# Optimization experiments

Hardware: AMD Instinct MI355X
Metric: run time of the kernel (lower is better)

The kernel has to match this reference:

```python
import jax, jax.numpy as jnp
import numpy as np

FEATURES = 4096
BATCH = 2048


def setup_inputs() -> dict:
    key = jax.random.key(0)
    kx, kk = jax.random.split(key)
    x = jax.random.normal(kx, (BATCH, FEATURES), dtype=jnp.float32)
    kernel = jax.random.normal(kk, (FEATURES,), dtype=jnp.float32)
    return {"x": x, "kernel": kernel}


def reference(x, kernel):
    n = kernel.shape[0]
    i = jnp.arange(n)[:, None]   # [n,1]
    j = jnp.arange(n)[None, :]   # [1,n]
    idx = i - j                   # Toeplitz offsets
    # W[i,j] = kernel[i-j] if i>=j else 0  (causal lower-triangular Toeplitz)
    W = jnp.where(idx >= 0, kernel[jnp.clip(idx, 0, n - 1)], 0.0)
    # out[b,i] = sum_{j<=i} x[b,j] * kernel[i-j]  == x @ W.T
    return x @ W.T
```

## Files before the change

### kernel.cpp

```cpp
#include <hip/hip_runtime.h>
#include <hip/hip_bf16.h>


typedef unsigned short u16;
typedef __attribute__((ext_vector_type(8))) short  bf16x8;
typedef __attribute__((ext_vector_type(8))) unsigned short u16x8;
typedef __attribute__((ext_vector_type(4))) float  f32x4;

#define KDIM 4096
#define NDIM 4096
#define MDIM 2048
#define KREV_STRIDE 4608
#define KREV_BYTES  (8 * KREV_STRIDE * 2)
#define BSTRIDE 456
#define BBUF    (8 * BSTRIDE)

static __device__ inline u16 f2bf(float f) {
  unsigned u = __builtin_bit_cast(unsigned, f);
  unsigned r = u + 0x7FFFu + ((u >> 16) & 1u);
  return (u16)(r >> 16);
}

static __device__ inline void async_copy16(const void* g, void* l) {
  __builtin_amdgcn_global_load_lds((const __attribute__((address_space(1))) void*)g,
                                   (__attribute__((address_space(3))) void*)l,
                                   16, 0, 0);
}

__global__ __launch_bounds__(256) void prep(const float* __restrict__ x,
                                            const float* __restrict__ kern,
                                            u16* __restrict__ xb,
                                            u16* __restrict__ krevs,
                                            int conv_blocks) {
  int kb = (int)blockIdx.x - conv_blocks;
  if (kb >= 0) {
    int u = kb * 256 + threadIdx.x;
    for (int a = 0; a < 8; ++a) {
      int t = u + a - 8;
      u16 v = 0;
      if (t >= 0 && t <= 4095) v = f2bf(kern[4095 - t]);
      krevs[a * KREV_STRIDE + u] = v;
    }
  } else {
    size_t i = ((size_t)blockIdx.x * 256 + threadIdx.x) * 8;
    const f32x4* p = (const f32x4*)(x + i);
    f32x4 v0 = p[0], v1 = p[1];
    u16x8 r;
    r[0] = f2bf(v0[0]); r[1] = f2bf(v0[1]); r[2] = f2bf(v0[2]); r[3] = f2bf(v0[3]);
    r[4] = f2bf(v1[0]); r[5] = f2bf(v1[1]); r[6] = f2bf(v1[2]); r[7] = f2bf(v1[3]);
    *(u16x8*)(xb + i) = r;
  }
}

template <bool CONV>
__global__ __launch_bounds__(512, 4) void toeplitz_gemm(const void* __restrict__ Av,
                                                        const u16* __restrict__ krevs,
                                                        float* __restrict__ out) {
  __shared__ __align__(16) char smem_raw[80128];
  u16*   A_all = (u16*)smem_raw;
  u16*   B_all = (u16*)(smem_raw + 65536);
  f32x4* ep    = (f32x4*)smem_raw;

  const int tid  = threadIdx.x;
  const int w    = tid >> 6;
  const int g    = w >> 2;
  const int wl   = w & 3;
  const int lane = tid & 63;
  const int lane16 = lane & 15;
  const int quad   = lane >> 4;
  const int wm = wl >> 1;
  const int wn = wl & 1;

  const int b  = (int)blockIdx.x;
  const int x_ = b & 7;
  const int jj = b >> 3;
  const int mt = x_ + 8 * (jj & 1);
  const int ct = 31 - (jj >> 1);
  const int n0 = ct * 128;
  const int m0 = mt * 128;
  const int W  = 3968 - n0;

  int boff[4];
  for (int fn = 0; fn < 4; ++fn) {
    int n_g = n0 + wn * 64 + fn * 16 + lane16;
    int s0  = 4095 - n_g + quad * 8;
    int a   = s0 & 7;
    boff[fn] = a * BSTRIDE + (s0 - a + 8 - W);
  }

  f32x4 acc[4][4] = {};
  const int srow8 = lane >> 3;
  const int ssrc  = ((lane & 7) ^ srow8) * 8;

  const u16*  xb = (const u16*)Av;
  const float* xf = (const float*)Av;

  auto stageA = [&](int t) {
    const int k0 = t * 128 + g * 64;
    u16* A_dst = A_all + (((g << 1) | (t & 1)) << 13);
    if constexpr (CONV) {
      int j    = tid & 255;
      int row  = j >> 1;
      int lh   = j & 1;
      for (int lc = 0; lc < 4; ++lc) {
        int l = lh * 4 + lc;
        int p = l ^ (row & 7);
        const f32x4* px = (const f32x4*)(xf + (size_t)(m0 + row) * KDIM + k0 + l * 8);
        f32x4 v0 = px[0], v1 = px[1];
        u16x8 r;
        r[0]=f2bf(v0[0]); r[1]=f2bf(v0[1]); r[2]=f2bf(v0[2]); r[3]=f2bf(v0[3]);
        r[4]=f2bf(v1[0]); r[5]=f2bf(v1[1]); r[6]=f2bf(v1[2]); r[7]=f2bf(v1[3]);
        *(u16x8*)(&A_dst[row * 64 + p * 8]) = r;
      }
    } else {
      for (int c = 0; c < 4; ++c) {
        int g8  = c * 4 + wl;
        int row = g8 * 8 + srow8;
        async_copy16(xb + (size_t)(m0 + row) * KDIM + k0 + ssrc,
                     &A_dst[g8 * 512]);
      }
    }
  };
  auto stageB = [&](int c) {
    if (lane < 56)
      async_copy16(krevs + w * KREV_STRIDE + W + c * 256 + (lane << 3),
                   &B_all[(c & 1) * BBUF + w * BSTRIDE]);
  };

  stageB(0);
  stageA(0);
  asm volatile("s_waitcnt vmcnt(0) lgkmcnt(0)" ::: "memory");
  __builtin_amdgcn_s_barrier();
  asm volatile("" ::: "memory");

  const int cmax = ct >> 1;
  for (int t = 0; ; ++t) {
    if (t < ct) {
      stageA(t + 1);
      if (!(t & 1) && ((t >> 1) + 1) <= cmax) stageB((t >> 1) + 1);
    }
    const u16* Bb  = B_all + ((t >> 1) & 1) * BBUF;
    const u16* A_g = A_all + (((g << 1) | (t & 1)) << 13);
    const int  ksl = (t & 1) * 128 + g * 64;
    for (int kk = 0; kk < 2; ++kk) {
      bf16x8 af[4];
      const int p = (kk * 4 + quad) ^ (lane16 & 7);
      for (int fm = 0; fm < 4; ++fm) {
        int row = wm * 64 + fm * 16 + lane16;
        af[fm] = *(const bf16x8*)(&A_g[row * 64 + p * 8]);
      }
      bf16x8 bf[4];
      for (int fn = 0; fn < 4; ++fn)
        bf[fn] = *(const bf16x8*)(&Bb[boff[fn] + ksl + kk * 32]);
      __builtin_amdgcn_s_setprio(1);
      for (int fm = 0; fm < 4; ++fm)
        for (int fn = 0; fn < 4; ++fn)
          acc[fm][fn] = __builtin_amdgcn_mfma_f32_16x16x32_bf16(af[fm], bf[fn], acc[fm][fn], 0, 0, 0);
      __builtin_amdgcn_s_setprio(0);
    }
    if (t == ct) break;
    asm volatile("s_waitcnt vmcnt(0) lgkmcnt(0)" ::: "memory");
    __builtin_amdgcn_s_barrier();
    asm volatile("" ::: "memory");
  }

  const int j = tid & 255;
  for (int r = 0; r < 2; ++r) {
    __syncthreads();
    if (g == 1) {
      for (int fm2 = 0; fm2 < 2; ++fm2)
        for (int fn = 0; fn < 4; ++fn)
          ep[j * 9 + fm2 * 4 + fn] = acc[r * 2 + fm2][fn];
    }
    __syncthreads();
    if (g == 0) {
      for (int fm2 = 0; fm2 < 2; ++fm2)
        for (int fn = 0; fn < 4; ++fn)
          acc[r * 2 + fm2][fn] += ep[j * 9 + fm2 * 4 + fn];
    }
  }

  if (g == 0) {
    for (int fm = 0; fm < 4; ++fm) {
      int row_base = m0 + wm * 64 + fm * 16 + quad * 4;
      for (int fn = 0; fn < 4; ++fn) {
        int col = n0 + wn * 64 + fn * 16 + lane16;
        for (int r = 0; r < 4; ++r)
          out[(size_t)(row_base + r) * NDIM + col] = acc[fm][fn][r];
      }
    }
  }
}

extern "C" void kernel_launch(void* const* d_in, const int* in_sizes, int n_in,
                              void* d_out, int out_size, void* d_ws, size_t ws_size,
                              hipStream_t stream) {
  const float* x    = (const float*)d_in[0];
  const float* kern = (const float*)d_in[1];
  float* out = (float*)d_out;

  u16* krevs = (u16*)d_ws;
  u16* xb    = (u16*)((char*)d_ws + KREV_BYTES);
  const size_t need_fast = (size_t)KREV_BYTES + (size_t)MDIM * KDIM * 2;

  if (ws_size >= need_fast) {
    prep<<<4096 + 18, 256, 0, stream>>>(x, kern, xb, krevs, 4096);
    toeplitz_gemm<false><<<512, 512, 0, stream>>>(xb, krevs, out);
  } else {
    prep<<<18, 256, 0, stream>>>(x, kern, xb, krevs, 0);
    toeplitz_gemm<true><<<512, 512, 0, stream>>>(x, krevs, out);
  }
}
```

Measured before the change: 120.3 us.

## Pre-swizzle x into MFMA fragment layout and load A directly from global

The prep kernel now writes bf16 x in a fragment-major order so each lane's 16-byte A operand is contiguous. The GEMM drops LDS staging of A and loads A fragments straight from global/L2 into registers. This shrinks shared memory, which can raise occupancy, and halves the barrier count by syncing only on B buffer swaps. Block-to-tile ordering also interleaves long and short causal tiles for load balance, and setprio is removed. The trade-off is that the global load latency of A is now exposed on every step without software prefetch.

```diff
diff --git a/kernel.cpp b/kernel.cpp
--- a/kernel.cpp
+++ b/kernel.cpp
@@ -15,6 +15,8 @@
 #define BSTRIDE 456
 #define BBUF    (8 * BSTRIDE)
 
+#define MFMA_BF16 __builtin_amdgcn_mfma_f32_16x16x32_bf16
+
 static __device__ inline u16 f2bf(float f) {
   unsigned u = __builtin_bit_cast(unsigned, f);
   unsigned r = u + 0x7FFFu + ((u >> 16) & 1u);
@@ -32,9 +34,9 @@
                                             u16* __restrict__ xb,
                                             u16* __restrict__ krevs,
                                             int conv_blocks) {
-  int kb = (int)blockIdx.x - conv_blocks;
-  if (kb >= 0) {
-    int u = kb * 256 + threadIdx.x;
+  int kblk = (int)blockIdx.x - conv_blocks;
+  if (kblk >= 0) {
+    int u = kblk * 256 + threadIdx.x;
     for (int a = 0; a < 8; ++a) {
       int t = u + a - 8;
       u16 v = 0;
@@ -42,13 +44,18 @@
       krevs[a * KREV_STRIDE + u] = v;
     }
   } else {
-    size_t i = ((size_t)blockIdx.x * 256 + threadIdx.x) * 8;
-    const f32x4* p = (const f32x4*)(x + i);
+    unsigned tg  = blockIdx.x * 256 + threadIdx.x;
+    unsigned l   = tg & 63;
+    unsigned kb  = (tg >> 6) & 127;
+    unsigned rg  = tg >> 13;
+    unsigned row = rg * 16 + (l & 15);
+    unsigned k   = kb * 32 + (l >> 4) * 8;
+    const f32x4* p = (const f32x4*)(x + (size_t)row * KDIM + k);
     f32x4 v0 = p[0], v1 = p[1];
     u16x8 r;
     r[0] = f2bf(v0[0]); r[1] = f2bf(v0[1]); r[2] = f2bf(v0[2]); r[3] = f2bf(v0[3]);
     r[4] = f2bf(v1[0]); r[5] = f2bf(v1[1]); r[6] = f2bf(v1[2]); r[7] = f2bf(v1[3]);
-    *(u16x8*)(xb + i) = r;
+    *(u16x8*)(xb + (size_t)tg * 8) = r;
   }
 }
 
@@ -56,9 +63,8 @@
 __global__ __launch_bounds__(512, 4) void toeplitz_gemm(const void* __restrict__ Av,
                                                         const u16* __restrict__ krevs,
                                                         float* __restrict__ out) {
-  __shared__ __align__(16) char smem_raw[80128];
-  u16*   A_all = (u16*)smem_raw;
-  u16*   B_all = (u16*)(smem_raw + 65536);
+  __shared__ __align__(16) char smem_raw[36864];
+  u16*   B_all = (u16*)smem_raw;
   f32x4* ep    = (f32x4*)smem_raw;
 
   const int tid  = threadIdx.x;
@@ -74,8 +80,10 @@
   const int b  = (int)blockIdx.x;
   const int x_ = b & 7;
   const int jj = b >> 3;
-  const int mt = x_ + 8 * (jj & 1);
-  const int ct = 31 - (jj >> 1);
+  const int q  = jj & 31;
+  const int h  = jj >> 5;
+  const int mt = x_ + 8 * (q & 1);
+  const int ct = h ? (q >> 1) : 31 - (q >> 1);
   const int n0 = ct * 128;
   const int m0 = mt * 128;
   const int W  = 3968 - n0;
@@ -89,38 +97,16 @@
   }
 
   f32x4 acc[4][4] = {};
-  const int srow8 = lane >> 3;
-  const int ssrc  = ((lane & 7) ^ srow8) * 8;
-
-  const u16*  xb = (const u16*)Av;
-  const float* xf = (const float*)Av;
-
-  auto stageA = [&](int t) {
-    const int k0 = t * 128 + g * 64;
-    u16* A_dst = A_all + (((g << 1) | (t & 1)) << 13);
-    if constexpr (CONV) {
-      int j    = tid & 255;
-      int row  = j >> 1;
-      int lh   = j & 1;
-      for (int lc = 0; lc < 4; ++lc) {
-        int l = lh * 4 + lc;
-        int p = l ^ (row & 7);
-        const f32x4* px = (const f32x4*)(xf + (size_t)(m0 + row) * KDIM + k0 + l * 8);
-        f32x4 v0 = px[0], v1 = px[1];
-        u16x8 r;
-        r[0]=f2bf(v0[0]); r[1]=f2bf(v0[1]); r[2]=f2bf(v0[2]); r[3]=f2bf(v0[3]);
-        r[4]=f2bf(v1[0]); r[5]=f2bf(v1[1]); r[6]=f2bf(v1[2]); r[7]=f2bf(v1[3]);
-        *(u16x8*)(&A_dst[row * 64 + p * 8]) = r;
-      }
-    } else {
-      for (int c = 0; c < 4; ++c) {
-        int g8  = c * 4 + wl;
-        int row = g8 * 8 + srow8;
-        async_copy16(xb + (size_t)(m0 + row) * KDIM + k0 + ssrc,
-                     &A_dst[g8 * 512]);
-      }
-    }
-  };
+
+  const u16*   xb2 = (const u16*)Av;
+  const float* xf  = (const float*)Av;
+  const u16* pA[4];
+  if constexpr (!CONV) {
+    for (int fm = 0; fm < 4; ++fm)
+      pA[fm] = xb2 + (size_t)(mt * 8 + wm * 4 + fm) * 65536 + g * 1024 + lane * 8;
+  }
+  const int rowb = m0 + wm * 64 + lane16;
+
   auto stageB = [&](int c) {
     if (lane < 56)
       async_copy16(krevs + w * KREV_STRIDE + W + c * 256 + (lane << 3),
@@ -128,40 +114,47 @@
   };
 
   stageB(0);
-  stageA(0);
   asm volatile("s_waitcnt vmcnt(0) lgkmcnt(0)" ::: "memory");
   __builtin_amdgcn_s_barrier();
   asm volatile("" ::: "memory");
 
   const int cmax = ct >> 1;
   for (int t = 0; ; ++t) {
-    if (t < ct) {
-      stageA(t + 1);
-      if (!(t & 1) && ((t >> 1) + 1) <= cmax) stageB((t >> 1) + 1);
-    }
+    if (!(t & 1) && ((t >> 1) + 1) <= cmax) stageB((t >> 1) + 1);
+
     const u16* Bb  = B_all + ((t >> 1) & 1) * BBUF;
-    const u16* A_g = A_all + (((g << 1) | (t & 1)) << 13);
     const int  ksl = (t & 1) * 128 + g * 64;
+#pragma unroll
     for (int kk = 0; kk < 2; ++kk) {
       bf16x8 af[4];
-      const int p = (kk * 4 + quad) ^ (lane16 & 7);
-      for (int fm = 0; fm < 4; ++fm) {
-        int row = wm * 64 + fm * 16 + lane16;
-        af[fm] = *(const bf16x8*)(&A_g[row * 64 + p * 8]);
+      if constexpr (!CONV) {
+        const int eo = t * 2048 + kk * 512;
+        for (int fm = 0; fm < 4; ++fm)
+          af[fm] = *(const bf16x8*)(pA[fm] + eo);
+      } else {
+        const int k0 = t * 128 + g * 64 + kk * 32 + quad * 8;
+        for (int fm = 0; fm < 4; ++fm) {
+          const f32x4* px = (const f32x4*)(xf + (size_t)(rowb + fm * 16) * KDIM + k0);
+          f32x4 v0 = px[0], v1 = px[1];
+          u16x8 r;
+          r[0]=f2bf(v0[0]); r[1]=f2bf(v0[1]); r[2]=f2bf(v0[2]); r[3]=f2bf(v0[3]);
+          r[4]=f2bf(v1[0]); r[5]=f2bf(v1[1]); r[6]=f2bf(v1[2]); r[7]=f2bf(v1[3]);
+          af[fm] = __builtin_bit_cast(bf16x8, r);
+        }
       }
-      bf16x8 bf[4];
+      bf16x8 bfr[4];
       for (int fn = 0; fn < 4; ++fn)
-        bf[fn] = *(const bf16x8*)(&Bb[boff[fn] + ksl + kk * 32]);
-      __builtin_amdgcn_s_setprio(1);
+        bfr[fn] = *(const bf16x8*)(&Bb[boff[fn] + ksl + kk * 32]);
       for (int fm = 0; fm < 4; ++fm)
         for (int fn = 0; fn < 4; ++fn)
-          acc[fm][fn] = __builtin_amdgcn_mfma_f32_16x16x32_bf16(af[fm], bf[fn], acc[fm][fn], 0, 0, 0);
-      __builtin_amdgcn_s_setprio(0);
+          acc[fm][fn] = MFMA_BF16(af[fm], bfr[fn], acc[fm][fn], 0, 0, 0);
     }
     if (t == ct) break;
-    asm volatile("s_waitcnt vmcnt(0) lgkmcnt(0)" ::: "memory");
-    __builtin_amdgcn_s_barrier();
-    asm volatile("" ::: "memory");
+    if (t & 1) {
+      asm volatile("s_waitcnt vmcnt(0) lgkmcnt(0)" ::: "memory");
+      __builtin_amdgcn_s_barrier();
+      asm volatile("" ::: "memory");
+    }
   }
 
   const int j = tid & 255;
```

Result: slower. 124.8 us (+3.7%).
